# Optimization experiments

Measured on AMD Instinct MI355X. Metric: run time of the kernel, lower is better.

The kernel has to match this reference:

```python
import jax, jax.numpy as jnp
import numpy as np

B, S, D, H = 4, 1024, 512, 16
HD = D // H
SCALE = 1.0 / np.sqrt(HD).astype(np.float32)


def setup_inputs() -> dict:
    key = jax.random.key(0)
    ks = jax.random.split(key, 20)
    std = 1.0 / np.sqrt(D).astype(np.float32)
    def W(k):
        return jax.random.normal(k, (D, D), jnp.float32) * std
    def b(k):
        return jax.random.normal(k, (D,), jnp.float32) * 0.01
    return {
        "x": jax.random.normal(ks[0], (B, S, D), jnp.float32),
        "ln_g": jnp.ones((D,), jnp.float32),
        "ln_b": jnp.zeros((D,), jnp.float32),
        "Wfa": W(ks[1]), "bfa": b(ks[2]),
        "Whp": W(ks[3]), "bhp": b(ks[4]),
        "Wmg": W(ks[5]), "bmg": b(ks[6]),
        "Wq": W(ks[7]), "bq": b(ks[8]),
        "Wk": W(ks[9]), "bk": b(ks[10]),
        "Wv": W(ks[11]), "bv": b(ks[12]),
        "Wo": W(ks[13]), "bo": b(ks[14]),
    }


def reference(x, ln_g, ln_b, Wfa, bfa, Whp, bhp, Wmg, bmg, Wq, bq, Wk, bk, Wv, bv, Wo, bo):
    residual = x
    # LayerNorm
    mu = jnp.mean(x, axis=-1, keepdims=True)
    var = jnp.mean(jnp.square(x - mu), axis=-1, keepdims=True)
    xn = (x - mu) * jax.lax.rsqrt(var + 1e-5) * ln_g + ln_b

    def lin(h, W, bb):
        return h @ W + bb

    fa = lin(xn, Wfa, bfa).reshape(B, S, H, HD)            # flow anchors, per-head
    hf = lin(xn, Whp, bhp).reshape(B, S, H, HD)            # hierarchical features
    mg = jax.nn.sigmoid(lin(xn, Wmg, bmg)).reshape(B, S, H, HD)  # memory gates
    q = lin(xn, Wq, bq).reshape(B, S, H, HD)
    k = lin(xn, Wk, bk).reshape(B, S, H, HD)
    v = lin(xn, Wv, bv).reshape(B, S, H, HD)

    # anchor weights: softmax over the SEQUENCE axis (dim=1)
    anchor_w = jax.nn.softmax(fa, axis=1)                  # [B,S,H,HD]
    k_weighted = k * anchor_w

    scores = jnp.einsum("bshd,bthd->bsht", q, k_weighted) * SCALE  # [B,S,H,T]
    probs = jax.nn.softmax(scores, axis=2)                 # softmax over HEAD axis (non-standard)
    attn = jnp.einsum("bsht,bthd->bshd", probs, v)         # [B,S,H,HD]

    out = (attn * mg + hf).reshape(B, S, D)
    out = lin(out, Wo, bo)
    return out + residual
```

## Files before the change

kernel.cpp:

```cpp
#include <hip/hip_runtime.h>
#include <hip/hip_bf16.h>
#include <math.h>

#define BB 4
#define SS 1024
#define DD 512
#define HH 16
#define HD 32
#define NTOK (BB * SS)
#define NELEM ((size_t)NTOK * DD)
#define SCALE 0.17677669529663687f
#define SCLOG2E 0.25505526082484745f

typedef __attribute__((ext_vector_type(8))) __bf16 bf16x8;
typedef __attribute__((ext_vector_type(4))) __bf16 bf16x4;
typedef __attribute__((ext_vector_type(4))) float f32x4;
typedef __attribute__((ext_vector_type(4))) unsigned short us4;

__device__ __forceinline__ void gload16(const void* g, void* l) {
    __builtin_amdgcn_global_load_lds(
        (const __attribute__((address_space(1))) void*)g,
        (__attribute__((address_space(3))) void*)l, 16, 0, 0);
}

__global__ __launch_bounds__(256) void ln_kernel(const float* __restrict__ x,
                                                 const float* __restrict__ g,
                                                 const float* __restrict__ bta,
                                                 __bf16* __restrict__ xn) {
    int row = blockIdx.x;
    int tid = threadIdx.x;
    const float* xr = x + (size_t)row * DD;
    float2 v = *reinterpret_cast<const float2*>(&xr[tid * 2]);
    float s1 = v.x + v.y;
    float s2 = v.x * v.x + v.y * v.y;
    for (int off = 32; off > 0; off >>= 1) {
        s1 += __shfl_down(s1, off);
        s2 += __shfl_down(s2, off);
    }
    __shared__ float r1[4], r2[4];
    int w = tid >> 6;
    if ((tid & 63) == 0) { r1[w] = s1; r2[w] = s2; }
    __syncthreads();
    s1 = r1[0] + r1[1] + r1[2] + r1[3];
    s2 = r2[0] + r2[1] + r2[2] + r2[3];
    float mu = s1 * (1.0f / DD);
    float var = s2 * (1.0f / DD) - mu * mu;
    float rstd = rsqrtf(var + 1e-5f);
    float2 gg = *reinterpret_cast<const float2*>(&g[tid * 2]);
    float2 bb = *reinterpret_cast<const float2*>(&bta[tid * 2]);
    __bf16* xp = xn + (size_t)row * DD + tid * 2;
    xp[0] = (__bf16)((v.x - mu) * rstd * gg.x + bb.x);
    xp[1] = (__bf16)((v.y - mu) * rstd * gg.y + bb.y);
}

struct W7 { const float* p[7]; };

__global__ __launch_bounds__(256) void wprep(W7 wp, __bf16* __restrict__ Wt) {
    int z = blockIdx.z;
    int kt = blockIdx.x, nt = blockIdx.y;
    const float* W = wp.p[z];
    __shared__ float lds[32][33];
    int tid = threadIdx.x;
    int r = tid >> 3, c4 = (tid & 7) * 4;
    float4 vv = *reinterpret_cast<const float4*>(W + (size_t)(kt * 32 + r) * DD + nt * 32 + c4);
    lds[r][c4 + 0] = vv.x; lds[r][c4 + 1] = vv.y;
    lds[r][c4 + 2] = vv.z; lds[r][c4 + 3] = vv.w;
    __syncthreads();
    __bf16* o = Wt + (size_t)z * DD * DD + (size_t)(nt * 32 + r) * DD + kt * 32 + c4;
    o[0] = (__bf16)lds[c4 + 0][r];
    o[1] = (__bf16)lds[c4 + 1][r];
    o[2] = (__bf16)lds[c4 + 2][r];
    o[3] = (__bf16)lds[c4 + 3][r];
}

struct GemmCfg { const float* bias[6]; void* out[6]; int mode[6]; };

__global__ __launch_bounds__(256) void mfma_gemm(const __bf16* __restrict__ A,
                                                 const __bf16* __restrict__ Wt0,
                                                 GemmCfg cfg,
                                                 const float* __restrict__ resid) {
    __shared__ __align__(16) char smem[24576];
    int z = blockIdx.z;
    const char* Ab8 = (const char*)A;
    const char* Bb8 = (const char*)(Wt0 + (size_t)z * DD * DD);
    int tid = threadIdx.x;
    int l = tid & 63, wid = tid >> 6;
    int lr = l & 15, lg = l >> 4;
    int wm = wid >> 1, wn = wid & 1;
    int bm = blockIdx.x * 128;
    int bn = blockIdx.y * 64;

    f32x4 acc[4][2];
#pragma unroll
    for (int i = 0; i < 4; ++i)
#pragma unroll
        for (int j = 0; j < 2; ++j) acc[i][j] = (f32x4){0.f, 0.f, 0.f, 0.f};

    for (int k0 = 0; k0 < DD; k0 += 64) {
#pragma unroll
        for (int i = 0; i < 4; ++i) {
            int r = wid * 32 + i * 8 + (l >> 3);
            int cb = ((l & 7) * 16) ^ ((r & 7) << 4);
            gload16(Ab8 + (size_t)(bm + r) * 1024 + k0 * 2 + cb,
                    smem + wid * 4096 + i * 1024);
        }
#pragma unroll
        for (int i = 0; i < 2; ++i) {
            int r = wid * 16 + i * 8 + (l >> 3);
            int cb = ((l & 7) * 16) ^ ((r & 7) << 4);
            gload16(Bb8 + (size_t)(bn + r) * 1024 + k0 * 2 + cb,
                    smem + 16384 + wid * 2048 + i * 1024);
        }
        asm volatile("s_waitcnt vmcnt(0)" ::: "memory");
        __syncthreads();

#pragma unroll
        for (int kk = 0; kk < 2; ++kk) {
            bf16x8 af[4], wf[2];
#pragma unroll
            for (int mi = 0; mi < 4; ++mi) {
                int m = wm * 64 + mi * 16 + lr;
                af[mi] = *reinterpret_cast<const bf16x8*>(
                    smem + m * 128 + ((kk * 64 + lg * 16) ^ ((m & 7) << 4)));
            }
#pragma unroll
            for (int ni = 0; ni < 2; ++ni) {
                int n = wn * 32 + ni * 16 + lr;
                wf[ni] = *reinterpret_cast<const bf16x8*>(
                    smem + 16384 + n * 128 + ((kk * 64 + lg * 16) ^ ((n & 7) << 4)));
            }
            __builtin_amdgcn_s_setprio(1);
#pragma unroll
            for (int mi = 0; mi < 4; ++mi)
#pragma unroll
                for (int ni = 0; ni < 2; ++ni)
                    acc[mi][ni] = __builtin_amdgcn_mfma_f32_16x16x32_bf16(af[mi], wf[ni], acc[mi][ni], 0, 0, 0);
            __builtin_amdgcn_s_setprio(0);
        }
        __syncthreads();
    }

    int bmw = bm + wm * 64;
    int bnw = bn + wn * 32;
    int mode = cfg.mode[z];
    const float* bias = cfg.bias[z];
    float bv[2] = {bias[bnw + lr], bias[bnw + 16 + lr]};
#pragma unroll
    for (int mi = 0; mi < 4; ++mi) {
#pragma unroll
        for (int ni = 0; ni < 2; ++ni) {
#pragma unroll
            for (int r = 0; r < 4; ++r) {
                int row = bmw + mi * 16 + lg * 4 + r;
                int col = bnw + ni * 16 + lr;
                float val = acc[mi][ni][r] + bv[ni];
                if (mode == 0) {
                    if (resid) val += resid[(size_t)row * DD + col];
                    ((float*)cfg.out[z])[(size_t)row * DD + col] = val;
                } else if (mode == 1) {
                    val = 1.0f / (1.0f + expf(-val));
                    ((__bf16*)cfg.out[z])[(size_t)row * DD + col] = (__bf16)val;
                } else {
                    ((__bf16*)cfg.out[z])[(size_t)row * DD + col] = (__bf16)val;
                }
            }
        }
    }
}

__global__ __launch_bounds__(256) void anchor_partial(const __bf16* __restrict__ fa,
                                                      float* __restrict__ pmax,
                                                      float* __restrict__ psum) {
    int tx = threadIdx.x;
    int ty = threadIdx.y;
    int c = blockIdx.x * 64 + tx;
    int b = blockIdx.y;
    int sc = blockIdx.z;
    const __bf16* base = fa + ((size_t)(b * SS + sc * 256)) * DD + c;
    float m = -1e30f;
    for (int i = ty; i < 256; i += 4) m = fmaxf(m, (float)base[(size_t)i * DD]);
    __shared__ float red[4][64];
    red[ty][tx] = m;
    __syncthreads();
    float cm = fmaxf(fmaxf(red[0][tx], red[1][tx]), fmaxf(red[2][tx], red[3][tx]));
    float s = 0.f;
    for (int i = ty; i < 256; i += 4) s += expf((float)base[(size_t)i * DD] - cm);
    __syncthreads();
    red[ty][tx] = s;
    __syncthreads();
    if (ty == 0) {
        float tot = red[0][tx] + red[1][tx] + red[2][tx] + red[3][tx];
        int o = (b * 4 + sc) * DD + c;
        pmax[o] = cm;
        psum[o] = tot;
    }
}

__global__ __launch_bounds__(256) void anchor_merge(const float* __restrict__ pmax,
                                                    const float* __restrict__ psum,
                                                    float2* __restrict__ smscale) {
    int idx = blockIdx.x * 256 + threadIdx.x;
    int b = idx >> 9;
    int c = idx & 511;
    float M = -1e30f;
#pragma unroll
    for (int j = 0; j < 4; ++j) M = fmaxf(M, pmax[(b * 4 + j) * DD + c]);
    float Z = 0.f;
#pragma unroll
    for (int j = 0; j < 4; ++j) Z += psum[(b * 4 + j) * DD + c] * expf(pmax[(b * 4 + j) * DD + c] - M);
    smscale[idx] = make_float2(M, 1.0f / Z);
}

__global__ __launch_bounds__(256) void kweight(const __bf16* __restrict__ fa,
                                               const __bf16* __restrict__ kin,
                                               const float2* __restrict__ sm,
                                               __bf16* __restrict__ kw) {
    size_t f = ((size_t)blockIdx.x * 256 + threadIdx.x) * 8;
    int b = (int)(f >> 19);
    int c = (int)(f & 511);
    bf16x8 fv = *reinterpret_cast<const bf16x8*>(fa + f);
    bf16x8 kv = *reinterpret_cast<const bf16x8*>(kin + f);
    const float2* smb = sm + b * DD + c;
    bf16x8 o;
#pragma unroll
    for (int j = 0; j < 8; ++j) {
        float2 s = smb[j];
        o[j] = (__bf16)((float)kv[j] * expf((float)fv[j] - s.x) * s.y);
    }
    *reinterpret_cast<bf16x8*>(kw + f) = o;
}

__global__ __launch_bounds__(256) void vtrans(const __bf16* __restrict__ v,
                                              __bf16* __restrict__ vt) {
    int t0 = blockIdx.x * 32;
    int h = blockIdx.y;
    int b = blockIdx.z;
    __shared__ unsigned short lds[32][33];
    int tid = threadIdx.x;
    int r = tid >> 3, c4 = (tid & 7) * 4;
    const unsigned short* vp = (const unsigned short*)v + ((size_t)(b * SS + t0 + r)) * DD + h * 32 + c4;
    us4 val = *reinterpret_cast<const us4*>(vp);
    lds[r][c4 + 0] = val[0]; lds[r][c4 + 1] = val[1];
    lds[r][c4 + 2] = val[2]; lds[r][c4 + 3] = val[3];
    __syncthreads();
    us4 o;
    o[0] = lds[c4 + 0][r]; o[1] = lds[c4 + 1][r];
    o[2] = lds[c4 + 2][r]; o[3] = lds[c4 + 3][r];
    unsigned short* op = (unsigned short*)vt +
        ((size_t)(b * 128 + ((t0 + c4) >> 3)) * 512 + h * 32 + r) * 8 + (c4 & 7);
    *reinterpret_cast<us4*>(op) = o;
}

struct P8 { __bf16* p[8]; };

__global__ __launch_bounds__(256) void attn_mfma(const __bf16* __restrict__ q,
                                                 const __bf16* __restrict__ kw,
                                                 const __bf16* __restrict__ vt,
                                                 P8 ps) {
    __shared__ __align__(16) char smem[65536];
    int sg = blockIdx.x;
    int b = blockIdx.y;
    int tp = blockIdx.z;
    int tid = threadIdx.x;
    int wid = tid >> 6;
    int lane = tid & 63;
    int lg = lane >> 4;
    int lr = lane & 15;
    int s0 = (sg * 4 + wid) * 16;

    const __bf16* qbase = q + ((size_t)(b * SS + s0 + lr)) * DD + lg * 8;
    const char* kwb8 = (const char*)kw + (size_t)b * SS * DD * 2;
    const char* vtb8 = (const char*)vt + (size_t)b * 128 * 8192;

    bf16x8 qf[16];
#pragma unroll
    for (int h = 0; h < 16; ++h) qf[h] = *reinterpret_cast<const bf16x8*>(qbase + h * 32);

    f32x4 acc[16][2];
#pragma unroll
    for (int h = 0; h < 16; ++h) {
        acc[h][0] = (f32x4){0.f, 0.f, 0.f, 0.f};
        acc[h][1] = (f32x4){0.f, 0.f, 0.f, 0.f};
    }

    int trowA = 8 * (lr >> 2) + (lr & 3);
    int trowB = trowA + 4;
    int xsl = lr << 4;

    for (int tc = 0; tc < 128; tc += 32) {
        int tbase = tp * 128 + tc;
#pragma unroll
        for (int it = 0; it < 8; ++it) {
            int row = it * 4 + wid;
            int colb = (lane * 16) ^ (((row & 3) << 4) | (((row >> 3) & 3) << 6));
            gload16(kwb8 + (size_t)(tbase + row) * 1024 + colb,
                    smem + it * 4096 + wid * 1024);
        }
#pragma unroll
        for (int it = 0; it < 8; ++it) {
            int blkid = it * 4 + wid;
            int lgq = blkid >> 3;
            gload16(vtb8 + (size_t)((tbase >> 3) + lgq) * 8192 + (blkid & 7) * 1024 + lane * 16,
                    smem + 32768 + it * 4096 + wid * 1024);
        }
        asm volatile("s_waitcnt vmcnt(0)" ::: "memory");
        __syncthreads();

        f32x4 sc[16];
#pragma unroll
        for (int hb = 0; hb < 16; hb += 4) {
            bf16x8 ka[4];
#pragma unroll
            for (int j = 0; j < 4; ++j) {
                int h = hb + j;
                ka[j] = *reinterpret_cast<const bf16x8*>(
                    smem + trowA * 1024 + ((h * 64 + lg * 16) ^ xsl));
            }
            __builtin_amdgcn_s_setprio(1);
#pragma unroll
            for (int j = 0; j < 4; ++j) {
                f32x4 z = (f32x4){0.f, 0.f, 0.f, 0.f};
                sc[hb + j] = __builtin_amdgcn_mfma_f32_16x16x32_bf16(ka[j], qf[hb + j], z, 0, 0, 0);
            }
            __builtin_amdgcn_s_setprio(0);
        }
        bf16x4 pA[16];
#pragma unroll
        for (int r = 0; r < 4; ++r) {
            float e[16]; float zs = 0.f;
#pragma unroll
            for (int h = 0; h < 16; ++h) { e[h] = exp2f(sc[h][r] * SCLOG2E); zs += e[h]; }
            float inv = __builtin_amdgcn_rcpf(zs);
#pragma unroll
            for (int h = 0; h < 16; ++h) pA[h][r] = (__bf16)(e[h] * inv);
        }
#pragma unroll
        for (int hb = 0; hb < 16; hb += 4) {
            bf16x8 ka[4];
#pragma unroll
            for (int j = 0; j < 4; ++j) {
                int h = hb + j;
                ka[j] = *reinterpret_cast<const bf16x8*>(
                    smem + trowB * 1024 + ((h * 64 + lg * 16) ^ xsl));
            }
            __builtin_amdgcn_s_setprio(1);
#pragma unroll
            for (int j = 0; j < 4; ++j) {
                f32x4 z = (f32x4){0.f, 0.f, 0.f, 0.f};
                sc[hb + j] = __builtin_amdgcn_mfma_f32_16x16x32_bf16(ka[j], qf[hb + j], z, 0, 0, 0);
            }
            __builtin_amdgcn_s_setprio(0);
        }
        bf16x4 pB[16];
#pragma unroll
        for (int r = 0; r < 4; ++r) {
            float e[16]; float zs = 0.f;
#pragma unroll
            for (int h = 0; h < 16; ++h) { e[h] = exp2f(sc[h][r] * SCLOG2E); zs += e[h]; }
            float inv = __builtin_amdgcn_rcpf(zs);
#pragma unroll
            for (int h = 0; h < 16; ++h) pB[h][r] = (__bf16)(e[h] * inv);
        }
#pragma unroll
        for (int hb = 0; hb < 16; hb += 4) {
            bf16x8 vf[8];
#pragma unroll
            for (int j = 0; j < 4; ++j) {
                int h = hb + j;
                vf[2 * j + 0] = *reinterpret_cast<const bf16x8*>(
                    smem + 32768 + lg * 8192 + h * 512 + lr * 16);
                vf[2 * j + 1] = *reinterpret_cast<const bf16x8*>(
                    smem + 32768 + lg * 8192 + h * 512 + 256 + lr * 16);
            }
            __builtin_amdgcn_s_setprio(1);
#pragma unroll
            for (int j = 0; j < 4; ++j) {
                int h = hb + j;
                bf16x8 p = __builtin_shufflevector(pA[h], pB[h], 0, 1, 2, 3, 4, 5, 6, 7);
                acc[h][0] = __builtin_amdgcn_mfma_f32_16x16x32_bf16(p, vf[2 * j + 0], acc[h][0], 0, 0, 0);
                acc[h][1] = __builtin_amdgcn_mfma_f32_16x16x32_bf16(p, vf[2 * j + 1], acc[h][1], 0, 0, 0);
            }
            __builtin_amdgcn_s_setprio(0);
        }
        __syncthreads();
    }

    __bf16* pb = ps.p[tp] + ((size_t)(b * SS + s0)) * DD;
#pragma unroll
    for (int h = 0; h < 16; ++h)
#pragma unroll
        for (int dh = 0; dh < 2; ++dh)
#pragma unroll
            for (int r = 0; r < 4; ++r)
                pb[(size_t)(lg * 4 + r) * DD + h * 32 + dh * 16 + lr] = (__bf16)acc[h][dh][r];
}

struct P8c { const __bf16* p[8]; };

__global__ __launch_bounds__(256) void combine_kernel(P8c ps,
                                                      const __bf16* __restrict__ mg,
                                                      const __bf16* __restrict__ hf,
                                                      __bf16* __restrict__ comb) {
    size_t f = ((size_t)blockIdx.x * 256 + threadIdx.x) * 8;
    float accv[8] = {0.f, 0.f, 0.f, 0.f, 0.f, 0.f, 0.f, 0.f};
#pragma unroll
    for (int i = 0; i < 8; ++i) {
        bf16x8 v = *reinterpret_cast<const bf16x8*>(ps.p[i] + f);
#pragma unroll
        for (int j = 0; j < 8; ++j) accv[j] += (float)v[j];
    }
    bf16x8 m = *reinterpret_cast<const bf16x8*>(mg + f);
    bf16x8 hh = *reinterpret_cast<const bf16x8*>(hf + f);
    bf16x8 o;
#pragma unroll
    for (int j = 0; j < 8; ++j) o[j] = (__bf16)(accv[j] * (float)m[j] + (float)hh[j]);
    *reinterpret_cast<bf16x8*>(comb + f) = o;
}

extern "C" void kernel_launch(void* const* d_in, const int* in_sizes, int n_in,
                              void* d_out, int out_size, void* d_ws, size_t ws_size,
                              hipStream_t stream) {
    const float* x    = (const float*)d_in[0];
    const float* ln_g = (const float*)d_in[1];
    const float* ln_b = (const float*)d_in[2];
    const float* Wfa  = (const float*)d_in[3];  const float* bfa = (const float*)d_in[4];
    const float* Whp  = (const float*)d_in[5];  const float* bhp = (const float*)d_in[6];
    const float* Wmg  = (const float*)d_in[7];  const float* bmg = (const float*)d_in[8];
    const float* Wq   = (const float*)d_in[9];  const float* bq  = (const float*)d_in[10];
    const float* Wk   = (const float*)d_in[11]; const float* bk  = (const float*)d_in[12];
    const float* Wv   = (const float*)d_in[13]; const float* bv  = (const float*)d_in[14];
    const float* Wo   = (const float*)d_in[15]; const float* bo  = (const float*)d_in[16];
    float* out = (float*)d_out;

    char* w8 = (char*)d_ws;
    __bf16* Wt   = (__bf16*)(w8 + ((size_t) 0 << 20));
    __bf16* xn   = (__bf16*)(w8 + ((size_t) 4 << 20));
    __bf16* fa   = (__bf16*)(w8 + ((size_t) 8 << 20));
    __bf16* hf   = (__bf16*)(w8 + ((size_t)12 << 20));
    __bf16* mg   = (__bf16*)(w8 + ((size_t)16 << 20));
    __bf16* q    = (__bf16*)(w8 + ((size_t)20 << 20));
    __bf16* k    = (__bf16*)(w8 + ((size_t)24 << 20));
    __bf16* v    = (__bf16*)(w8 + ((size_t)28 << 20));
    __bf16* kw   = (__bf16*)(w8 + ((size_t)32 << 20));
    __bf16* vt   = (__bf16*)(w8 + ((size_t)36 << 20));
    P8 ps;
    ps.p[0] = (__bf16*)(w8 + ((size_t) 4 << 20));
    ps.p[1] = (__bf16*)(w8 + ((size_t) 8 << 20));
    ps.p[2] = (__bf16*)(w8 + ((size_t)24 << 20));
    ps.p[3] = (__bf16*)(w8 + ((size_t)28 << 20));
    ps.p[4] = (__bf16*)(w8 + ((size_t)40 << 20));
    ps.p[5] = (__bf16*)(w8 + ((size_t)44 << 20));
    ps.p[6] = (__bf16*)(w8 + ((size_t)48 << 20));
    ps.p[7] = (__bf16*)(w8 + ((size_t)52 << 20));
    __bf16* comb = (__bf16*)(w8 + ((size_t)56 << 20));
    float* pmax  = (float*) (w8 + ((size_t)60 << 20));
    float* psum  = pmax + 16 * DD;
    float2* smsc = (float2*)(psum + 16 * DD);

    ln_kernel<<<NTOK, 256, 0, stream>>>(x, ln_g, ln_b, xn);

    W7 wp; wp.p[0]=Wfa; wp.p[1]=Whp; wp.p[2]=Wmg; wp.p[3]=Wq; wp.p[4]=Wk; wp.p[5]=Wv; wp.p[6]=Wo;
    wprep<<<dim3(16, 16, 7), 256, 0, stream>>>(wp, Wt);

    GemmCfg cfg;
    cfg.bias[0]=bfa; cfg.out[0]=fa; cfg.mode[0]=2;
    cfg.bias[1]=bhp; cfg.out[1]=hf; cfg.mode[1]=2;
    cfg.bias[2]=bmg; cfg.out[2]=mg; cfg.mode[2]=1;
    cfg.bias[3]=bq;  cfg.out[3]=q;  cfg.mode[3]=2;
    cfg.bias[4]=bk;  cfg.out[4]=k;  cfg.mode[4]=2;
    cfg.bias[5]=bv;  cfg.out[5]=v;  cfg.mode[5]=2;
    mfma_gemm<<<dim3(32, 8, 6), 256, 0, stream>>>(xn, Wt, cfg, nullptr);

    anchor_partial<<<dim3(8, 4, 4), dim3(64, 4), 0, stream>>>(fa, pmax, psum);
    anchor_merge<<<8, 256, 0, stream>>>(pmax, psum, smsc);
    kweight<<<1024, 256, 0, stream>>>(fa, k, smsc, kw);

    vtrans<<<dim3(32, 16, 4), 256, 0, stream>>>(v, vt);

    attn_mfma<<<dim3(16, 4, 8), 256, 0, stream>>>(q, kw, vt, ps);

    P8c pc;
    for (int i = 0; i < 8; ++i) pc.p[i] = ps.p[i];
    combine_kernel<<<1024, 256, 0, stream>>>(pc, mg, hf, comb);

    GemmCfg cfg2;
    for (int i = 0; i < 6; ++i) { cfg2.bias[i]=bo; cfg2.out[i]=out; cfg2.mode[i]=0; }
    mfma_gemm<<<dim3(32, 8, 1), 256, 0, stream>>>(comb, Wt + (size_t)6 * DD * DD, cfg2, x);
}
```

Before: 148.8 us.

## Prefetch next K/V tiles during attention compute and fold softmax scale into Q

The attention loop now issues the next chunk's K-weighted tile load right after the score/softmax phase, and the next V tile after the PV MFMAs. Partial vmcnt waits and split barriers replace the single full wait and syncthreads, so global-to-LDS transfers overlap with compute instead of stalling each iteration. Separately, the Q projection epilogue pre-multiplies by scale*log2e, which removes a multiply per exp in the head softmax. The price is finer-grained synchronisation that depends on the LDS reuse ordering being correct, and Q is rounded to bf16 after scaling, which slightly changes numerics.

```diff
diff --git a/kernel.cpp b/kernel.cpp
--- a/kernel.cpp
+++ b/kernel.cpp
@@ -160,6 +160,8 @@
                 } else if (mode == 1) {
                     val = 1.0f / (1.0f + expf(-val));
                     ((__bf16*)cfg.out[z])[(size_t)row * DD + col] = (__bf16)val;
+                } else if (mode == 3) {
+                    ((__bf16*)cfg.out[z])[(size_t)row * DD + col] = (__bf16)(val * SCLOG2E);
                 } else {
                     ((__bf16*)cfg.out[z])[(size_t)row * DD + col] = (__bf16)val;
                 }
@@ -287,8 +289,7 @@
     int trowB = trowA + 4;
     int xsl = lr << 4;
 
-    for (int tc = 0; tc < 128; tc += 32) {
-        int tbase = tp * 128 + tc;
+    auto stage_kw = [&](int tbase) {
 #pragma unroll
         for (int it = 0; it < 8; ++it) {
             int row = it * 4 + wid;
@@ -296,6 +297,8 @@
             gload16(kwb8 + (size_t)(tbase + row) * 1024 + colb,
                     smem + it * 4096 + wid * 1024);
         }
+    };
+    auto stage_vt = [&](int tbase) {
 #pragma unroll
         for (int it = 0; it < 8; ++it) {
             int blkid = it * 4 + wid;
@@ -303,8 +306,17 @@
             gload16(vtb8 + (size_t)((tbase >> 3) + lgq) * 8192 + (blkid & 7) * 1024 + lane * 16,
                     smem + 32768 + it * 4096 + wid * 1024);
         }
-        asm volatile("s_waitcnt vmcnt(0)" ::: "memory");
-        __syncthreads();
+    };
+
+    int tbase0 = tp * 128;
+    stage_kw(tbase0);
+    stage_vt(tbase0);
+
+    for (int tc = 0; tc < 128; tc += 32) {
+        int tbase = tbase0 + tc;
+        asm volatile("s_waitcnt vmcnt(8)" ::: "memory");
+        __builtin_amdgcn_s_barrier();
+        __builtin_amdgcn_sched_barrier(0);
 
         f32x4 sc[16];
 #pragma unroll
@@ -329,7 +341,7 @@
         for (int r = 0; r < 4; ++r) {
             float e[16]; float zs = 0.f;
 #pragma unroll
-            for (int h = 0; h < 16; ++h) { e[h] = exp2f(sc[h][r] * SCLOG2E); zs += e[h]; }
+            for (int h = 0; h < 16; ++h) { e[h] = exp2f(sc[h][r]); zs += e[h]; }
             float inv = __builtin_amdgcn_rcpf(zs);
 #pragma unroll
             for (int h = 0; h < 16; ++h) pA[h][r] = (__bf16)(e[h] * inv);
@@ -356,11 +368,22 @@
         for (int r = 0; r < 4; ++r) {
             float e[16]; float zs = 0.f;
 #pragma unroll
-            for (int h = 0; h < 16; ++h) { e[h] = exp2f(sc[h][r] * SCLOG2E); zs += e[h]; }
+            for (int h = 0; h < 16; ++h) { e[h] = exp2f(sc[h][r]); zs += e[h]; }
             float inv = __builtin_amdgcn_rcpf(zs);
 #pragma unroll
             for (int h = 0; h < 16; ++h) pB[h][r] = (__bf16)(e[h] * inv);
         }
+
+        __builtin_amdgcn_s_barrier();
+        if (tc + 32 < 128) {
+            stage_kw(tbase + 32);
+            asm volatile("s_waitcnt vmcnt(8)" ::: "memory");
+        } else {
+            asm volatile("s_waitcnt vmcnt(0)" ::: "memory");
+        }
+        __builtin_amdgcn_s_barrier();
+        __builtin_amdgcn_sched_barrier(0);
+
 #pragma unroll
         for (int hb = 0; hb < 16; hb += 4) {
             bf16x8 vf[8];
@@ -382,7 +405,9 @@
             }
             __builtin_amdgcn_s_setprio(0);
         }
-        __syncthreads();
+
+        __builtin_amdgcn_s_barrier();
+        if (tc + 32 < 128) stage_vt(tbase + 32);
     }
 
     __bf16* pb = ps.p[tp] + ((size_t)(b * SS + s0)) * DD;
@@ -466,7 +491,7 @@
     cfg.bias[0]=bfa; cfg.out[0]=fa; cfg.mode[0]=2;
     cfg.bias[1]=bhp; cfg.out[1]=hf; cfg.mode[1]=2;
     cfg.bias[2]=bmg; cfg.out[2]=mg; cfg.mode[2]=1;
-    cfg.bias[3]=bq;  cfg.out[3]=q;  cfg.mode[3]=2;
+    cfg.bias[3]=bq;  cfg.out[3]=q;  cfg.mode[3]=3;
     cfg.bias[4]=bk;  cfg.out[4]=k;  cfg.mode[4]=2;
     cfg.bias[5]=bv;  cfg.out[5]=v;  cfg.mode[5]=2;
     mfma_gemm<<<dim3(32, 8, 6), 256, 0, stream>>>(xn, Wt, cfg, nullptr);
```

Measured after the change: 152.7 us. 1.03x slower.

## Shrink attention t-chunk to 16 and fold softmax scale into Q projection

Applied to the files above, without the earlier changes.

Each iteration of the attention kernel now covers 16 keys instead of 32, which halves its shared memory use (32KB instead of 64KB) and should allow more blocks per CU. The PV product uses the 16x16x16 bf16 MFMA with 4-element operands, and the K tile gets a simpler XOR swizzle. The softmax scale times log2(e) is now applied in the Q GEMM epilogue, so the per-score multiply before exp2 goes away. The cost is twice as many loop iterations and barriers, smaller MFMAs with less work per instruction, and Q rounded to bf16 after scaling.

```diff
diff --git a/kernel.cpp b/kernel.cpp
--- a/kernel.cpp
+++ b/kernel.cpp
@@ -16,6 +16,7 @@
 typedef __attribute__((ext_vector_type(4))) __bf16 bf16x4;
 typedef __attribute__((ext_vector_type(4))) float f32x4;
 typedef __attribute__((ext_vector_type(4))) unsigned short us4;
+typedef __attribute__((ext_vector_type(4))) short s16x4;
 
 __device__ __forceinline__ void gload16(const void* g, void* l) {
     __builtin_amdgcn_global_load_lds(
@@ -160,6 +161,8 @@
                 } else if (mode == 1) {
                     val = 1.0f / (1.0f + expf(-val));
                     ((__bf16*)cfg.out[z])[(size_t)row * DD + col] = (__bf16)val;
+                } else if (mode == 3) {
+                    ((__bf16*)cfg.out[z])[(size_t)row * DD + col] = (__bf16)(val * SCLOG2E);
                 } else {
                     ((__bf16*)cfg.out[z])[(size_t)row * DD + col] = (__bf16)val;
                 }
@@ -257,7 +260,7 @@
                                                  const __bf16* __restrict__ kw,
                                                  const __bf16* __restrict__ vt,
                                                  P8 ps) {
-    __shared__ __align__(16) char smem[65536];
+    __shared__ __align__(16) char smem[32768];
     int sg = blockIdx.x;
     int b = blockIdx.y;
     int tp = blockIdx.z;
@@ -283,25 +286,21 @@
         acc[h][1] = (f32x4){0.f, 0.f, 0.f, 0.f};
     }
 
-    int trowA = 8 * (lr >> 2) + (lr & 3);
-    int trowB = trowA + 4;
-    int xsl = lr << 4;
-
-    for (int tc = 0; tc < 128; tc += 32) {
+    for (int tc = 0; tc < 128; tc += 16) {
         int tbase = tp * 128 + tc;
 #pragma unroll
-        for (int it = 0; it < 8; ++it) {
+        for (int it = 0; it < 4; ++it) {
             int row = it * 4 + wid;
-            int colb = (lane * 16) ^ (((row & 3) << 4) | (((row >> 3) & 3) << 6));
+            int colb = (lane * 16) ^ ((row & 7) << 4);
             gload16(kwb8 + (size_t)(tbase + row) * 1024 + colb,
-                    smem + it * 4096 + wid * 1024);
-        }
-#pragma unroll
-        for (int it = 0; it < 8; ++it) {
+                    smem + row * 1024);
+        }
+#pragma unroll
+        for (int it = 0; it < 4; ++it) {
             int blkid = it * 4 + wid;
             int lgq = blkid >> 3;
             gload16(vtb8 + (size_t)((tbase >> 3) + lgq) * 8192 + (blkid & 7) * 1024 + lane * 16,
-                    smem + 32768 + it * 4096 + wid * 1024);
+                    smem + 16384 + blkid * 1024);
         }
         asm volatile("s_waitcnt vmcnt(0)" ::: "memory");
         __syncthreads();
@@ -314,7 +313,7 @@
             for (int j = 0; j < 4; ++j) {
                 int h = hb + j;
                 ka[j] = *reinterpret_cast<const bf16x8*>(
-                    smem + trowA * 1024 + ((h * 64 + lg * 16) ^ xsl));
+                    smem + lr * 1024 + ((h * 64 + lg * 16) ^ ((lr & 7) << 4)));
             }
             __builtin_amdgcn_s_setprio(1);
 #pragma unroll
@@ -329,56 +328,28 @@
         for (int r = 0; r < 4; ++r) {
             float e[16]; float zs = 0.f;
 #pragma unroll
-            for (int h = 0; h < 16; ++h) { e[h] = exp2f(sc[h][r] * SCLOG2E); zs += e[h]; }
+            for (int h = 0; h < 16; ++h) { e[h] = exp2f(sc[h][r]); zs += e[h]; }
             float inv = __builtin_amdgcn_rcpf(zs);
 #pragma unroll
             for (int h = 0; h < 16; ++h) pA[h][r] = (__bf16)(e[h] * inv);
         }
 #pragma unroll
         for (int hb = 0; hb < 16; hb += 4) {
-            bf16x8 ka[4];
+            s16x4 vf[8];
 #pragma unroll
             for (int j = 0; j < 4; ++j) {
                 int h = hb + j;
-                ka[j] = *reinterpret_cast<const bf16x8*>(
-                    smem + trowB * 1024 + ((h * 64 + lg * 16) ^ xsl));
+                const char* vb = smem + 16384 + (lg >> 1) * 8192 + (lg & 1) * 8;
+                vf[2 * j + 0] = *reinterpret_cast<const s16x4*>(vb + (h * 32 + lr) * 16);
+                vf[2 * j + 1] = *reinterpret_cast<const s16x4*>(vb + (h * 32 + 16 + lr) * 16);
             }
             __builtin_amdgcn_s_setprio(1);
-#pragma unroll
-            for (int j = 0; j < 4; ++j) {
-                f32x4 z = (f32x4){0.f, 0.f, 0.f, 0.f};
-                sc[hb + j] = __builtin_amdgcn_mfma_f32_16x16x32_bf16(ka[j], qf[hb + j], z, 0, 0, 0);
-            }
-            __builtin_amdgcn_s_setprio(0);
-        }
-        bf16x4 pB[16];
-#pragma unroll
-        for (int r = 0; r < 4; ++r) {
-            float e[16]; float zs = 0.f;
-#pragma unroll
-            for (int h = 0; h < 16; ++h) { e[h] = exp2f(sc[h][r] * SCLOG2E); zs += e[h]; }
-            float inv = __builtin_amdgcn_rcpf(zs);
-#pragma unroll
-            for (int h = 0; h < 16; ++h) pB[h][r] = (__bf16)(e[h] * inv);
-        }
-#pragma unroll
-        for (int hb = 0; hb < 16; hb += 4) {
-            bf16x8 vf[8];
 #pragma unroll
             for (int j = 0; j < 4; ++j) {
                 int h = hb + j;
-                vf[2 * j + 0] = *reinterpret_cast<const bf16x8*>(
-                    smem + 32768 + lg * 8192 + h * 512 + lr * 16);
-                vf[2 * j + 1] = *reinterpret_cast<const bf16x8*>(
-                    smem + 32768 + lg * 8192 + h * 512 + 256 + lr * 16);
-            }
-            __builtin_amdgcn_s_setprio(1);
-#pragma unroll
-            for (int j = 0; j < 4; ++j) {
-                int h = hb + j;
-                bf16x8 p = __builtin_shufflevector(pA[h], pB[h], 0, 1, 2, 3, 4, 5, 6, 7);
-                acc[h][0] = __builtin_amdgcn_mfma_f32_16x16x32_bf16(p, vf[2 * j + 0], acc[h][0], 0, 0, 0);
-                acc[h][1] = __builtin_amdgcn_mfma_f32_16x16x32_bf16(p, vf[2 * j + 1], acc[h][1], 0, 0, 0);
+                s16x4 pa = __builtin_bit_cast(s16x4, pA[h]);
+                acc[h][0] = __builtin_amdgcn_mfma_f32_16x16x16bf16_1k(pa, vf[2 * j + 0], acc[h][0], 0, 0, 0);
+                acc[h][1] = __builtin_amdgcn_mfma_f32_16x16x16bf16_1k(pa, vf[2 * j + 1], acc[h][1], 0, 0, 0);
             }
             __builtin_amdgcn_s_setprio(0);
         }
@@ -466,7 +437,7 @@
     cfg.bias[0]=bfa; cfg.out[0]=fa; cfg.mode[0]=2;
     cfg.bias[1]=bhp; cfg.out[1]=hf; cfg.mode[1]=2;
     cfg.bias[2]=bmg; cfg.out[2]=mg; cfg.mode[2]=1;
-    cfg.bias[3]=bq;  cfg.out[3]=q;  cfg.mode[3]=2;
+    cfg.bias[3]=bq;  cfg.out[3]=q;  cfg.mode[3]=3;
     cfg.bias[4]=bk;  cfg.out[4]=k;  cfg.mode[4]=2;
     cfg.bias[5]=bv;  cfg.out[5]=v;  cfg.mode[5]=2;
     mfma_gemm<<<dim3(32, 8, 6), 256, 0, stream>>>(xn, Wt, cfg, nullptr);
```

Result: slower. 155.9 us (+4.8%).
